# Performance work log

Measured on AMD Instinct MI355X. Metric: run time of the kernel, lower is better.

## Reference

```python
import jax, jax.numpy as jnp
import numpy as np
from math import ceil

N, C_IN, HV, WV = 4, 3, 256, 256
C, K, NUM_LAYERS = 16, 3, 10
HK, WK = 45, 45
PROX_SCALE, KSCALE, KBSCALE, EPS = 10.0, 100.0, 0.01, 1e-8


def conv2_same(x, w):
    # torch F.conv2d (cross-correlation) with 'same' padding
    return jax.lax.conv_general_dilated(x, w, (1, 1), 'SAME',
                                        dimension_numbers=('NCHW', 'OIHW', 'NCHW'))


def pad_to(x, size):
    h, w = x.shape[-2], x.shape[-1]
    pads = [(0, 0)] * (x.ndim - 2) + [(0, size[0] - h), (0, size[1] - w)]
    return jnp.pad(x, pads)


def soft_threshold(x, b):
    return jnp.sign(x) * jax.nn.relu(jnp.abs(x) - b)


def circ_shift(x, s):
    return jnp.roll(x, (-s[0], -s[1]), axis=(-2, -1))


def csq(c):
    return (c * jnp.conj(c)).real


def forward(blurred_image, w0, ws, biases, kernel_biases, kernel_proxes, zetas, eta):
    Nb, C_in, Hv, Wv = blurred_image.shape
    Hs, Ws = Hv + HK - 1, Wv + WK - 1
    Hb, Wb = Hs + HK - 1, Ws + WK - 1
    fft_size = (int(ceil(Hb / 64.0) * 64), int(ceil(Wb / 64.0) * 64))
    rfft = lambda x: jnp.fft.rfft2(x, s=fft_size, axes=(-2, -1))
    irfft = lambda X: jnp.fft.irfft2(X, s=fft_size, axes=(-2, -1))

    # first-layer filter: zero-mean per (out,in) filter, then spatial reflect
    w_mean = w0.reshape(C, C_in, -1).mean(axis=-1)
    w0c = w0 - w_mean[:, :, None, None]
    w0_unreflected = jnp.transpose(w0c, (1, 0, 2, 3))   # (C_in, C, K, K)
    w0r = w0c[:, :, ::-1, ::-1]

    # analysis: cascade of convs, each feature stack padded to fft_size
    wy_list = []
    fy = blurred_image
    for layer in range(NUM_LAYERS):
        w = w0r if layer == 0 else ws[layer - 1]
        fy = conv2_same(fy, w)
        fy_p = pad_to(jnp.pad(fy, ((0, 0), (0, 0), (HK - 1, HK - 1), (WK - 1, WK - 1))), fft_size)
        wy_list.append(fy_p)

    delta = jnp.zeros((Nb, HK, WK), dtype=blurred_image.dtype).at[:, HK // 2, WK // 2].set(1.0)
    b0 = biases[0][None, :, None, None]
    z = soft_threshold(circ_shift(wy_list[-1], (HK // 2, WK // 2)), b0)
    Fz = rfft(z)
    k = delta
    Fg = None
    for layer in range(NUM_LAYERS):
        fy_p = wy_list.pop()
        Ffy = rfft(fy_p)                       # (N, C, H, Wf) complex
        Fk = rfft(k)[:, None]                  # (N, 1, H, Wf)
        zeta = PROX_SCALE * zetas[layer][None, :, None, None]
        num = zeta * (jnp.conj(Fk) * Ffy) + Fz
        den = zeta * csq(Fk) + 1.0
        Fg = num / (den + EPS)
        b = biases[layer + 1][None, :, None, None]
        z = soft_threshold(irfft(Fg), b)
        Fz = rfft(z)
        zk = kernel_proxes[layer]
        num_k = zk * jnp.sum(jnp.conj(Fz) * Ffy, axis=1) + Fk[:, 0]
        den_k = zk * jnp.sum(csq(Fz), axis=1) + 1.0
        k = irfft(num_k / (den_k + EPS))
        k_flat = k.reshape(Nb, -1)
        k_max = jax.scipy.special.logsumexp(k_flat * KSCALE, axis=-1) / KSCALE
        bk = KBSCALE * kernel_biases[layer]
        k = jax.nn.relu(k[:, :HK, :WK] - bk * k_max[:, None, None])
        k_sum = jnp.sum(k, axis=(1, 2), keepdims=True)
        k = (k + EPS * delta) / (k_sum + EPS)

    # final closed-form image solve in frequency domain (3-channel Cramer's rule)
    Fy = rfft(jnp.pad(blurred_image, ((0, 0), (0, 0), (HK - 1, HK - 1), (WK - 1, WK - 1))))
    Fk = rfft(k)                                # (N, H, Wf)
    Fw0 = rfft(circ_shift(pad_to(w0_unreflected, fft_size), (K // 2, K // 2)))  # (C_in, C, H, Wf)
    b_final = biases[NUM_LAYERS + 1][None, :, None, None]
    Fg = rfft(soft_threshold(irfft(Fg), b_final))

    eta_s = PROX_SCALE * eta[None, :, None, None]      # (1, C, 1, 1)
    Fwr, Fwg, Fwb = Fw0[0:1], Fw0[1:2], Fw0[2:3]       # (1, C, H, Wf)
    Fyr, Fyg, Fyb = Fy[:, 0], Fy[:, 1], Fy[:, 2]
    Fk_sq = csq(Fk)
    Crr = Fk_sq + jnp.sum(eta_s * csq(Fwr), axis=1)
    Cgg = Fk_sq + jnp.sum(eta_s * csq(Fwg), axis=1)
    Cbb = Fk_sq + jnp.sum(eta_s * csq(Fwb), axis=1)
    Crg = jnp.sum(eta_s * jnp.conj(Fwr) * Fwg, axis=1)
    Crb = jnp.sum(eta_s * jnp.conj(Fwr) * Fwb, axis=1)
    Cgb = jnp.sum(eta_s * jnp.conj(Fwg) * Fwb, axis=1)
    Fk_conj = jnp.conj(Fk)
    Br = Fk_conj * Fyr + jnp.sum(eta_s * jnp.conj(Fwr) * Fg, axis=1)
    Bg = Fk_conj * Fyg + jnp.sum(eta_s * jnp.conj(Fwg) * Fg, axis=1)
    Bb = Fk_conj * Fyb + jnp.sum(eta_s * jnp.conj(Fwb) * Fg, axis=1)
    Crg_sq, Crb_sq, Cgb_sq = csq(Crg), csq(Crb), csq(Cgb)
    Irr = Cgg * Cbb - Cgb_sq
    Igg = Crr * Cbb - Crb_sq
    Ibb = Crr * Cgg - Crg_sq
    Irg = jnp.conj(Cgb) * Crb - Cbb * Crg
    Irb = Crg * Cgb - Cgg * Crb
    Igb = jnp.conj(Crg) * Crb - Crr * Cgb
    den = (Crr * (Cgg * Cbb - Cgb_sq) - Cgg * Crb_sq - Cbb * Crg_sq
           + 2 * (Crg * Cgb * jnp.conj(Crb)).real) + EPS
    Fxr = Irr * Br + Irg * Bg + Irb * Bb
    Fxg = jnp.conj(Irg) * Br + Igg * Bg + Igb * Bb
    Fxb = jnp.conj(Irb) * Br + jnp.conj(Igb) * Bg + Ibb * Bb
    Fx = jnp.stack([Fxr, Fxg, Fxb], axis=1) / den[:, None]

    image = irfft(Fx)[:, :, HK // 2:HK // 2 + Hv, WK // 2:WK // 2 + Wv]
    return image, k


def setup_inputs() -> dict:
    key = jax.random.key(0)
    ks = jax.random.split(key, 4)

    def xavier(k, shape, fan_in, fan_out):
        std = (2.0 / (fan_in + fan_out)) ** 0.5
        return std * jax.random.normal(k, shape, dtype=jnp.float32)

    return {
        'blurred_image': jax.random.normal(ks[0], (N, C_IN, HV, WV), dtype=jnp.float32),
        'w0': xavier(ks[1], (C, C_IN, K, K), C_IN * K * K, C * K * K),
        'ws': xavier(ks[2], (NUM_LAYERS - 1, C, C, 3, 3), C * 9, C * 9),
        'biases': jnp.full((NUM_LAYERS + 2, C), 0.02, dtype=jnp.float32),
        'kernel_biases': jnp.zeros((NUM_LAYERS,), dtype=jnp.float32),
        'kernel_proxes': jnp.ones((NUM_LAYERS,), dtype=jnp.float32),
        'zetas': jnp.ones((NUM_LAYERS, C), dtype=jnp.float32),
        'eta': jnp.ones((C,), dtype=jnp.float32),
    }


def reference(blurred_image, w0, ws, biases, kernel_biases, kernel_proxes, zetas, eta):
    return forward(blurred_image, w0, ws, biases, kernel_biases, kernel_proxes, zetas, eta)
```

## Files before the change

kernel.cpp:

```cpp
#include <hip/hip_runtime.h>
#include <math.h>

#define FH 384
#define KF 193
#define SPW 147456

typedef __attribute__((ext_vector_type(8))) short short8;
typedef __attribute__((ext_vector_type(4))) float f32x4;
typedef unsigned int u32;
typedef unsigned short u16;

static __device__ __forceinline__ float softt(float v, float b) {
    return copysignf(fmaxf(fabsf(v) - b, 0.f), v);
}
static __device__ __forceinline__ u16 bf16_rn(float v) {
    u32 u = __float_as_uint(v);
    u32 r = (u + 0x7FFFu + ((u >> 16) & 1u)) >> 16;
    return (u16)r;
}
static __device__ __forceinline__ float bf16_to_f(u16 h) {
    return __uint_as_float(((u32)h) << 16);
}
static __device__ __forceinline__ float2 ldc(const uint2* __restrict__ S, size_t i) {
    uint2 u = S[i];
// ... 141 lines not shown
                v = inF ? inF[ii] : (bf16_to_f(iH[ii]) + bf16_to_f(iL[ii]));
            }
            tile[yy][xx] = v;
        }
        __syncthreads();
        float v[9];
#pragma unroll
        for (int dy = 0; dy < 3; dy++)
#pragma unroll
            for (int dx = 0; dx < 3; dx++) v[dy*3+dx] = tile[ty+dy][tx+dx];
#pragma unroll
        for (int co = 0; co < 16; co++) {
            const float* wp = &wl[(co*Cin+ci)*9];
            acc[co] += v[0]*wp[0]+v[1]*wp[1]+v[2]*wp[2]
                     + v[3]*wp[3]+v[4]*wp[4]+v[5]*wp[5]
                     + v[6]*wp[6]+v[7]*wp[7]+v[8]*wp[8];
        }
    }
    int xo = x0 + tx;
    int xd = (xo >> 1) + (xo & 1)*128;
#pragma unroll
    for (int co = 0; co < 16; co++) {
        size_t o = ((size_t)co*256 + (y0+ty))*256 + xd;
        u16 h = bf16_rn(acc[co]);
        oH[o] = h;
        oL[o] = bf16_rn(acc[co] - bf16_to_f(h));
    }
}

__global__ void zinit_kernel(const u16* __restrict__ fy9H, const u16* __restrict__ fy9L,
                             const float* __restrict__ b0,
                             u16* __restrict__ oH, u16* __restrict__ oL, int total)
{
    int idx = blockIdx.x*256 + threadIdx.x;
    if (idx >= total) return;
    int x = idx % FH; int r = idx / FH; int y = r % FH; int plane = r / FH;
    int c = plane & 15;
    int Y = y + 22; if (Y >= FH) Y -= FH;
    int X = x + 22; if (X >= FH) X -= FH;
    int yy = Y - 44, xx = X - 44;
    float v = 0.f;
    if (yy >= 0 && yy < 256 && xx >= 0 && xx < 256) {
        size_t ii = ((size_t)plane*256 + yy)*256 + ((xx>>1) + (xx&1)*128);
        v = bf16_to_f(fy9H[ii]) + bf16_to_f(fy9L[ii]);
    }
    float s = softt(v, b0[c]);
    u16 h = bf16_rn(s);
    size_t d = (size_t)plane*SPW + (size_t)y*FH + ((x>>1) + (x&1)*192);
    oH[d] = h;
    oL[d] = bf16_rn(s - bf16_to_f(h));
}

static __device__ __forceinline__ void r2c192_epilogue(
    f32x4 accA[2][4], f32x4 accB[2][4],
    int col0, int njN, int y0, int wave, int lm, int lq,
    const float2* __restrict__ twT,
    uint2* __restrict__ outp, int B, int plane)
{
#pragma unroll
    for (int mi = 0; mi < 2; ++mi) {
#pragma unroll
        for (int nj = 0; nj < 4; ++nj) {
            if (nj >= njN) continue;
            int n = col0 + nj*16 + lm;
            int j = n >> 1;
            float pA[4], pB[4];
#pragma unroll
            for (int rr = 0; rr < 4; ++rr) {
                pA[rr] = __shfl_xor(accA[mi][nj][rr], 1);
                pB[rr] = __shfl_xor(accB[mi][nj][rr], 1);
            }
            if (((lm & 1) == 0) && j <= 96) {
                float2 tw = twT[j];
                float wr = tw.x, wi = -tw.y;
                int ybase = y0 + wave*32 + mi*16 + lq*4;
#pragma unroll
                for (int rr = 0; rr < 4; ++rr) {
                    float ar = accA[mi][nj][rr], ai = pA[rr];
                    float br = accB[mi][nj][rr], bi = pB[rr];
                    float tr = wr*br - wi*bi;
                    float ti = wr*bi + wi*br;
                    size_t rowb = ((size_t)(ybase+rr)*B + plane)*KF;
                    outp[rowb + j] = packc(ar + tr, ai + ti);
                    if (j < 96) outp[rowb + 192 - j] = packc(ar - tr, -(ai - ti));
                }
            }
        }
    }
}

__global__ __launch_bounds__(256) void r2c192_f(
    const float* __restrict__ inp, int inH, int inW, int inStride, size_t planeStride,
    int offY, int offX,
    const float* __restrict__ thr,
    const u16* __restrict__ TH, const u16* __restrict__ TL,
    const float2* __restrict__ twT,
    uint2* __restrict__ outp, int B)
{
    __shared__ u16 AhS[2][8*64*8];
    __shared__ u16 AlS[2][8*64*8];
    int col0 = blockIdx.x * 64;
    int y0   = blockIdx.y * 128;
    int plane = blockIdx.z;
    int njN = (col0 >= 192) ? 1 : 4;
    int tid = threadIdx.x;
    int wave = tid >> 6, lane = tid & 63;
    int lm = lane & 15, lq = lane >> 4;
    f32x4 accA[2][4], accB[2][4];
#pragma unroll
    for (int mi = 0; mi < 2; ++mi)
#pragma unroll
        for (int nj = 0; nj < 4; ++nj) {
            accA[mi][nj] = (f32x4){0.f,0.f,0.f,0.f};
            accB[mi][nj] = (f32x4){0.f,0.f,0.f,0.f};
        }
    float bthr = thr ? thr[plane & 15] : 0.f;
    const float* inpP = inp + (size_t)plane*planeStride;
    int mhi = (offX + inW) >> 1;
    for (int kt = 0; kt < mhi; kt += 32) {
#pragma unroll
        for (int s = 0; s < 4; ++s) {
            int slot = tid + s*256;
            int r = slot >> 3, kq = slot & 7;
            int yy = y0 + r - offY;
            int xx0 = 2*(kt + kq*4) - offX;
            float v[8];
#pragma unroll
            for (int d = 0; d < 8; ++d) {
                int xx = xx0 + d;
                float t = 0.f;
                if (yy >= 0 && yy < inH && xx >= 0 && xx < inW)
                    t = inpP[(size_t)yy*inStride + xx];
                if (thr) t = softt(t, bthr);
                v[d] = t;
            }
            u16 h[8], l[8];
#pragma unroll
            for (int d = 0; d < 8; ++d) {
                h[d] = bf16_rn(v[d]);
                l[d] = bf16_rn(v[d] - bf16_to_f(h[d]));
            }
            int base = ((r >> 4)*64 + (r & 15) + 16*(kq >> 1))*8 + (kq & 1)*4;
            uint2 w;
            w.x = (u32)h[0] | ((u32)h[2] << 16); w.y = (u32)h[4] | ((u32)h[6] << 16);
            *(uint2*)&AhS[0][base] = w;
            w.x = (u32)h[1] | ((u32)h[3] << 16); w.y = (u32)h[5] | ((u32)h[7] << 16);
            *(uint2*)&AhS[1][base] = w;
            w.x = (u32)l[0] | ((u32)l[2] << 16); w.y = (u32)l[4] | ((u32)l[6] << 16);
            *(uint2*)&AlS[0][base] = w;
            w.x = (u32)l[1] | ((u32)l[3] << 16); w.y = (u32)l[5] | ((u32)l[7] << 16);
            *(uint2*)&AlS[1][base] = w;
        }
        __syncthreads();
        short8 A0h[2], A0l[2], A1h[2], A1l[2];
#pragma unroll
        for (int mi = 0; mi < 2; ++mi) {
            int fo = ((wave*2 + mi)*64 + lane)*8;
            A0h[mi] = *(const short8*)&AhS[0][fo];
            A0l[mi] = *(const short8*)&AlS[0][fo];
            A1h[mi] = *(const short8*)&AhS[1][fo];
            A1l[mi] = *(const short8*)&AlS[1][fo];
        }
#pragma unroll
        for (int nj = 0; nj < 4; ++nj) {
            if (nj >= njN) continue;
            size_t toff = (size_t)(col0 + nj*16 + lm)*192 + kt + lq*8;
            short8 Bh = *(const short8*)(TH + toff);
            short8 Bl = *(const short8*)(TL + toff);
#pragma unroll
            for (int mi = 0; mi < 2; ++mi) {
                accA[mi][nj] = __builtin_amdgcn_mfma_f32_16x16x32_bf16(A0h[mi], Bh, accA[mi][nj], 0, 0, 0);
                accA[mi][nj] = __builtin_amdgcn_mfma_f32_16x16x32_bf16(A0h[mi], Bl, accA[mi][nj], 0, 0, 0);
                accA[mi][nj] = __builtin_amdgcn_mfma_f32_16x16x32_bf16(A0l[mi], Bh, accA[mi][nj], 0, 0, 0);
                accB[mi][nj] = __builtin_amdgcn_mfma_f32_16x16x32_bf16(A1h[mi], Bh, accB[mi][nj], 0, 0, 0);
                accB[mi][nj] = __builtin_amdgcn_mfma_f32_16x16x32_bf16(A1h[mi], Bl, accB[mi][nj], 0, 0, 0);
                accB[mi][nj] = __builtin_amdgcn_mfma_f32_16x16x32_bf16(A1l[mi], Bh, accB[mi][nj], 0, 0, 0);
            }
        }
        __syncthreads();
    }
    r2c192_epilogue(accA, accB, col0, njN, y0, wave, lm, lq, twT, outp, B, plane);
}

__global__ __launch_bounds__(256) void r2c192_s(
    const u16* __restrict__ Hs, const u16* __restrict__ Ls,
    int inH, int inW, int offY, int offX,
    const u16* __restrict__ TH, const u16* __restrict__ TL,
    const float2* __restrict__ twT,
    uint2* __restrict__ outp, int B)
{
    __shared__ u16 AhS[2][8*64*8];
    __shared__ u16 AlS[2][8*64*8];
    int col0 = blockIdx.x * 64;
    int y0   = blockIdx.y * 128;
    int plane = blockIdx.z;
    int njN = (col0 >= 192) ? 1 : 4;
    int tid = threadIdx.x;
    int wave = tid >> 6, lane = tid & 63;
    int lm = lane & 15, lq = lane >> 4;
    f32x4 accA[2][4], accB[2][4];
#pragma unroll
    for (int mi = 0; mi < 2; ++mi)
#pragma unroll
        for (int nj = 0; nj < 4; ++nj) {
            accA[mi][nj] = (f32x4){0.f,0.f,0.f,0.f};
            accB[mi][nj] = (f32x4){0.f,0.f,0.f,0.f};
        }
    const u16* hP = Hs + (size_t)plane*inH*inW;
    const u16* lP = Ls + (size_t)plane*inH*inW;
    int W2  = inW >> 1;
    int ox2 = offX >> 1;
    bool al16 = ((ox2 & 7) == 0);
    int mhi = (offX + inW) >> 1;
    for (int kt = 0; kt < mhi; kt += 32) {
#pragma unroll
        for (int s = 0; s < 4; ++s) {
            int slot = tid + s*256;
            int p    = slot >> 9;
            int inr  = slot & 511;
            int r = inr >> 2, kq2 = inr & 3;
            int yy = y0 + r - offY;
            int m0 = kt + kq2*8;
            int pos = m0 - ox2;
            uint4 hq = {0u,0u,0u,0u}, lq4 = {0u,0u,0u,0u};
            if (yy >= 0 && yy < inH) {
                const u16* hr = hP + (size_t)yy*inW + (size_t)p*W2;
                const u16* lr = lP + (size_t)yy*inW + (size_t)p*W2;
                if (pos >= 0 && pos + 8 <= W2) {
                    if (al16) {
                        hq  = *(const uint4*)(hr + pos);
                        lq4 = *(const uint4*)(lr + pos);
                    } else {
                        hq.x = *(const u32*)(hr+pos);   hq.y = *(const u32*)(hr+pos+2);
                        hq.z = *(const u32*)(hr+pos+4); hq.w = *(const u32*)(hr+pos+6);
                        lq4.x = *(const u32*)(lr+pos);   lq4.y = *(const u32*)(lr+pos+2);
                        lq4.z = *(const u32*)(lr+pos+4); lq4.w = *(const u32*)(lr+pos+6);
                    }
                } else if (pos + 8 > 0 && pos < W2) {
#pragma unroll
                    for (int q = 0; q < 4; ++q) {
                        int pp = pos + 2*q;
                        if (pp >= 0 && pp + 2 <= W2) {
                            ((u32*)&hq)[q]  = *(const u32*)(hr+pp);
                            ((u32*)&lq4)[q] = *(const u32*)(lr+pp);
                        }
                    }
                }
            }
            int base = ((r >> 4)*64 + (r & 15) + 16*kq2)*8;
            *(uint4*)&AhS[p][base] = hq;
            *(uint4*)&AlS[p][base] = lq4;
        }
        __syncthreads();
        short8 A0h[2], A0l[2], A1h[2], A1l[2];
#pragma unroll
        for (int mi = 0; mi < 2; ++mi) {
            int fo = ((wave*2 + mi)*64 + lane)*8;
            A0h[mi] = *(const short8*)&AhS[0][fo];
            A0l[mi] = *(const short8*)&AlS[0][fo];
            A1h[mi] = *(const short8*)&AhS[1][fo];
            A1l[mi] = *(const short8*)&AlS[1][fo];
        }
#pragma unroll
        for (int nj = 0; nj < 4; ++nj) {
            if (nj >= njN) continue;
            size_t toff = (size_t)(col0 + nj*16 + lm)*192 + kt + lq*8;
            short8 Bh = *(const short8*)(TH + toff);
            short8 Bl = *(const short8*)(TL + toff);
#pragma unroll
            for (int mi = 0; mi < 2; ++mi) {
                accA[mi][nj] = __builtin_amdgcn_mfma_f32_16x16x32_bf16(A0h[mi], Bh, accA[mi][nj], 0, 0, 0);
                accA[mi][nj] = __builtin_amdgcn_mfma_f32_16x16x32_bf16(A0h[mi], Bl, accA[mi][nj], 0, 0, 0);
                accA[mi][nj] = __builtin_amdgcn_mfma_f32_16x16x32_bf16(A0l[mi], Bh, accA[mi][nj], 0, 0, 0);
                accB[mi][nj] = __builtin_amdgcn_mfma_f32_16x16x32_bf16(A1h[mi], Bh, accB[mi][nj], 0, 0, 0);
                accB[mi][nj] = __builtin_amdgcn_mfma_f32_16x16x32_bf16(A1h[mi], Bl, accB[mi][nj], 0, 0, 0);
                accB[mi][nj] = __builtin_amdgcn_mfma_f32_16x16x32_bf16(A1l[mi], Bh, accB[mi][nj], 0, 0, 0);
            }
        }
        __syncthreads();
    }
    r2c192_epilogue(accA, accB, col0, njN, y0, wave, lm, lq, twT, outp, B, plane);
}

__device__ __forceinline__ void lse_comb(float& m, float& s, float m2, float s2)
{
    if (m2 > m) { s = s * expf(m - m2) + s2; m = m2; }
    else        { s = s + s2 * expf(m2 - m); }
}

__global__ void gpm_kernel(uint2* __restrict__ S, const float2* __restrict__ twT, int rows)
{
    int idx = blockIdx.x*256 + threadIdx.x;
    if (idx >= rows * 97) return;
    int j = idx % 97;
    size_t b = (size_t)(idx / 97) * KF;
    if (j == 96) {
        float2 f = ldc(S, b + 96);
        S[b + 96] = packc(2.f*f.x, -2.f*f.y);
    } else {
        float2 f1 = ldc(S, b + j);
        float2 f2 = ldc(S, b + 192 - j);
        float gpx = f1.x + f2.x, gpy = f1.y - f2.y;
        float hx  = f1.x - f2.x, hy  = f1.y + f2.y;
        float2 tw = twT[j];
        float gmx = tw.x*hx - tw.y*hy;
        float gmy = tw.x*hy + tw.y*hx;
        S[b + j]       = packc(gpx, gpy);
        S[b + 192 - j] = packc(gmx, gmy);
    }
}

template<bool FUSE_LSE>
__global__ __launch_bounds__(256) void c2r192(
    const uint2* __restrict__ Ain,
    const u16* __restrict__ UH, const u16* __restrict__ UL,
    float* __restrict__ outp, const float* __restrict__ thr,
    u16* __restrict__ spH, u16* __restrict__ spL, int B,
    float2* __restrict__ parts)
{
    __shared__ u16 AhS[2][8*64*8];
    __shared__ u16 AlS[2][8*64*8];
    int col0 = blockIdx.x * 64;
    int y0   = blockIdx.y * 128;
    int plane = blockIdx.z;
    int tid = threadIdx.x;
    int wave = tid >> 6, lane = tid & 63;
    int lm = lane & 15, lq = lane >> 4;
    f32x4 accP[2][4], accQ[2][4];
#pragma unroll
    for (int mi = 0; mi < 2; ++mi)
#pragma unroll
        for (int nj = 0; nj < 4; ++nj) {
            accP[mi][nj] = (f32x4){0.f,0.f,0.f,0.f};
            accQ[mi][nj] = (f32x4){0.f,0.f,0.f,0.f};
        }
    for (int kt = 0; kt < 194; kt += 32) {
#pragma unroll
        for (int s = 0; s < 8; ++s) {
            int slot = tid + s*256;
            int p   = slot >> 10;
            int inr = slot & 1023;
            int r = inr >> 3, kq = inr & 7;
            size_t rowb = ((size_t)(y0 + r)*B + plane)*KF;
            int j0 = (kt + kq*4) >> 1;
            uint2 u0, u1;
            u0.x = u0.y = u1.x = u1.y = 0u;
            if (p == 0) {
                if (j0 < 96) u0 = Ain[rowb + j0];
                else if (j0 == 96) {
                    uint2 t = Ain[rowb + 96];
                    u0.x = t.x & 0xffffu; u0.y = t.y & 0xffffu;
                }
                if (j0 + 1 < 96) u1 = Ain[rowb + j0 + 1];
            } else {
                if (j0 < 96) u0 = Ain[rowb + 192 - j0];
                else if (j0 == 96) {
                    uint2 t = Ain[rowb + 96];
                    u0.x = t.x >> 16; u0.y = t.y >> 16;
                }
                if (j0 + 1 < 96) u1 = Ain[rowb + 191 - j0];
            }
            int base = ((r >> 4)*64 + (r & 15) + 16*(kq >> 1))*8 + (kq & 1)*4;
            uint2 hp, lp;
            hp.x = u0.x; hp.y = u1.x;
            lp.x = u0.y; lp.y = u1.y;
            *(uint2*)&AhS[p][base] = hp;
            *(uint2*)&AlS[p][base] = lp;
        }
        __syncthreads();
        short8 A0h[2], A0l[2], A1h[2], A1l[2];
#pragma unroll
        for (int mi = 0; mi < 2; ++mi) {
            int fo = ((wave*2 + mi)*64 + lane)*8;
            A0h[mi] = *(const short8*)&AhS[0][fo];
            A0l[mi] = *(const short8*)&AlS[0][fo];
            A1h[mi] = *(const short8*)&AhS[1][fo];
            A1l[mi] = *(const short8*)&AlS[1][fo];
        }
#pragma unroll
        for (int nj = 0; nj < 4; ++nj) {
            size_t toff = (size_t)(col0 + nj*16 + lm)*224 + kt + lq*8;
            short8 Bh = *(const short8*)(UH + toff);
            short8 Bl = *(const short8*)(UL + toff);
#pragma unroll
            for (int mi = 0; mi < 2; ++mi) {
                accP[mi][nj] = __builtin_amdgcn_mfma_f32_16x16x32_bf16(A0h[mi], Bh, accP[mi][nj], 0, 0, 0);
                accP[mi][nj] = __builtin_amdgcn_mfma_f32_16x16x32_bf16(A0h[mi], Bl, accP[mi][nj], 0, 0, 0);
                accP[mi][nj] = __builtin_amdgcn_mfma_f32_16x16x32_bf16(A0l[mi], Bh, accP[mi][nj], 0, 0, 0);
                accQ[mi][nj] = __builtin_amdgcn_mfma_f32_16x16x32_bf16(A1h[mi], Bh, accQ[mi][nj], 0, 0, 0);
                accQ[mi][nj] = __builtin_amdgcn_mfma_f32_16x16x32_bf16(A1h[mi], Bl, accQ[mi][nj], 0, 0, 0);
                accQ[mi][nj] = __builtin_amdgcn_mfma_f32_16x16x32_bf16(A1l[mi], Bh, accQ[mi][nj], 0, 0, 0);
            }
        }
        __syncthreads();
    }
    float bthr = thr ? thr[plane & 15] : 0.f;
    float lm_ = -1e30f, ls_ = 0.f;
#pragma unroll
    for (int mi = 0; mi < 2; ++mi) {
#pragma unroll
        for (int nj = 0; nj < 4; ++nj) {
            int m = col0 + nj*16 + lm;
#pragma unroll
            for (int rr = 0; rr < 4; ++rr) {
                int y = y0 + wave*32 + mi*16 + lq*4 + rr;
                float xe = accP[mi][nj][rr];
                float xo = accQ[mi][nj][rr];
                float2 o2; o2.x = xe; o2.y = xo;
                *(float2*)&outp[((size_t)plane*FH + y)*FH + 2*m] = o2;
                if (spH) {
                    float s0 = softt(xe, bthr), s1 = softt(xo, bthr);
                    u16 h0 = bf16_rn(s0), h1 = bf16_rn(s1);
                    u16 l0 = bf16_rn(s0 - bf16_to_f(h0)), l1 = bf16_rn(s1 - bf16_to_f(h1));
                    size_t d = (size_t)plane*SPW + (size_t)y*FH + m;
                    spH[d]       = h0; spL[d]       = l0;
                    spH[d + 192] = h1; spL[d + 192] = l1;
                }
                if (FUSE_LSE) {
                    lse_comb(lm_, ls_, 100.f*xe, 1.f);
                    lse_comb(lm_, ls_, 100.f*xo, 1.f);
                }
            }
        }
    }
    if (FUSE_LSE) {
        __shared__ float sm[256], ss[256];
        sm[tid] = lm_; ss[tid] = ls_;
        __syncthreads();
        for (int st = 128; st > 0; st >>= 1) {
            if (tid < st) {
                float mm = sm[tid], sc = ss[tid];
                lse_comb(mm, sc, sm[tid+st], ss[tid+st]);
                sm[tid] = mm; ss[tid] = sc;
            }
            __syncthreads();
        }
        if (tid == 0) {
            float2 o; o.x = sm[0]; o.y = ss[0];
            parts[plane*9 + blockIdx.y*3 + blockIdx.x] = o;
        }
    }
}

template<bool FUSE_FG>
__global__ __launch_bounds__(384) void zgemm_col_mfma8(
    const u16* __restrict__ EH, const u16* __restrict__ EL,
    const uint2* __restrict__ Bm, uint2* __restrict__ Cm, int N, float sgn,
    int ktHi, const float2* __restrict__ twT,
    uint2* __restrict__ FzFg, const uint2* __restrict__ FkB,
    const float* __restrict__ zet16, int GKF)
{
    __shared__ u16 BhS[8][2*64*8];
    __shared__ u16 BlS[8][2*64*8];
    int col0 = blockIdx.x * 32;
    int tid = threadIdx.x;
    int wave = tid >> 6, lane = tid & 63;
    int lm = lane & 15, lq = lane >> 4;
    f32x4 acc[8][2];
#pragma unroll
    for (int p = 0; p < 8; ++p)
#pragma unroll
        for (int nj = 0; nj < 2; ++nj)
            acc[p][nj] = (f32x4){0.f,0.f,0.f,0.f};
    int arow = wave*16 + lm;
    for (int kt = 0; kt < ktHi; kt += 32) {
        int tbase = kt >> 1;
#pragma unroll
        for (int s = 0; s < 6; ++s) {
            int slot = tid + s*384;
            if (slot < 2048) {
                int p    = slot >> 8;
                int inr  = slot & 255;
                int pair = inr >> 5;
                int n    = inr & 31;
                int gn   = col0 + n;
                int t0   = tbase + pair*2;
                uint2 u0, u1;
                u0.x = u0.y = u1.x = u1.y = 0u;
                if (gn < N) {
                    u0 = Bm[(size_t)(8*t0 + p)*N + gn];
                    u1 = Bm[(size_t)(8*t0 + 8 + p)*N + gn];
                }
                int ntile = n >> 4, n0 = n & 15;
                int lrow  = (pair >> 1)*16 + n0;
                int base  = (ntile*64 + lrow)*8 + (pair & 1)*4;
                uint2 hp, lp;
                hp.x = u0.x; hp.y = u1.x;
                lp.x = u0.y; lp.y = u1.y;
                *(uint2*)&BhS[p][base] = hp;
                *(uint2*)&BlS[p][base] = lp;
            }
        }
// ... 92 lines not shown
                        float den = zeta*(fk.x*fk.x + fk.y*fk.y) + 1.f + 1e-8f;
                        float inv = 1.f/den;
                        FzFg[(size_t)row*N + coln] = packc(nx*inv, ny*inv);
                    }
                }
            }
        }
    }
}

__global__ void knum_kernel(const uint2* __restrict__ Fz, const uint2* __restrict__ Ffy,
                            const uint2* __restrict__ Fk, const float* __restrict__ kprox,
                            int L, int total, uint2* __restrict__ outk)
{
    int idx = blockIdx.x*256 + threadIdx.x;
    if (idx >= total) return;
    int k = idx % KF; int r = idx / KF;
    float zk = kprox[L];
    float s1x = 0.f, s1y = 0.f, s2 = 0.f;
    for (int c = 0; c < 16; ++c) {
        size_t bi = ((size_t)r*16 + c)*KF + k;
        float2 fz = ldc(Fz, bi), fy = ldc(Ffy, bi);
        s1x += fz.x*fy.x + fz.y*fy.y;
        s1y += fz.x*fy.y - fz.y*fy.x;
        s2  += fz.x*fz.x + fz.y*fz.y;
    }
    float2 fk = ldc(Fk, idx);
    float nx = zk*s1x + fk.x, ny = zk*s1y + fk.y;
    float den = zk*s2 + 1.f + 1e-8f;
    float inv = 1.f/den;
    outk[idx] = packc(nx*inv, ny*inv);
}

__global__ void zero_kernel(float* __restrict__ p, int n)
{
    int i = blockIdx.x*256 + threadIdx.x;
    if (i < n) p[i] = 0.f;
}

__global__ void kdelta_kernel(float* __restrict__ kful, int G)
{
    int t = threadIdx.x;
    if (t < G) kful[(size_t)t*FH*FH + 22*FH + 22] = 1.f;
}

__global__ __launch_bounds__(256) void knew_kernel(const float2* __restrict__ parts,
    const float* __restrict__ kraw0, const float* __restrict__ kb, int L,
    float* __restrict__ kful0)
{
    int img = blockIdx.x;
    const float* kraw = kraw0 + (size_t)img*FH*FH;
    float*       kful = kful0 + (size_t)img*FH*FH;
    int t = threadIdx.x;
    __shared__ float sm[16], ss[16];
    if (t < 16) {
        if (t < 9) { float2 p = parts[img*9 + t]; sm[t] = p.x; ss[t] = p.y; }
        else       { sm[t] = -1e30f; ss[t] = 0.f; }
    }
    __syncthreads();
    for (int st = 8; st > 0; st >>= 1) {
        if (t < st) {
            float mm = sm[t], sc = ss[t];
            lse_comb(mm, sc, sm[t+st], ss[t+st]);
            sm[t] = mm; ss[t] = sc;
        }
        __syncthreads();
    }
    float kmax = (sm[0] + logf(ss[0])) * 0.01f;
    float thr = 0.01f * kb[L] * kmax;
    float vs[8]; float loc = 0.f;
#pragma unroll
    for (int ii = 0; ii < 8; ++ii) {
        int i = t + ii*256;
        float v = 0.f;
        if (i < 45*45) {
            int y = i/45, x = i - y*45;
            v = fmaxf(kraw[y*FH + x] - thr, 0.f);
        }
        vs[ii] = v; loc += v;
    }
    __shared__ float sr[256];
    sr[t] = loc; __syncthreads();
    for (int st = 128; st > 0; st >>= 1) { if (t < st) sr[t] += sr[t+st]; __syncthreads(); }
    float den = sr[0] + 1e-8f;
#pragma unroll
    for (int ii = 0; ii < 8; ++ii) {
        int i = t + ii*256;
        if (i < 45*45) {
            int y = i/45, x = i - y*45;
            float v = vs[ii] + ((y == 22 && x == 22) ? 1e-8f : 0.f);
            kful[y*FH + x] = v / den;
        }
    }
}

__global__ void fw0_kernel(const float* __restrict__ w0c, const float2* __restrict__ Ef,
                           float2* __restrict__ Fw0)
{
    int idx = blockIdx.x*256 + threadIdx.x;
    if (idx >= 48*FH*KF) return;
    int k = idx % KF; int r = idx / KF;
    int c = r & 15; int r2 = r >> 4;
    int ci = r2 % 3; int h = r2 / 3;
    float accx = 0.f, accy = 0.f;
#pragma unroll
    for (int ky = 0; ky < 3; ++ky) {
        int a1 = ky - 1; if (a1 < 0) a1 += FH;
        float2 e1 = Ef[h*FH + a1];
#pragma unroll
        for (int kx = 0; kx < 3; ++kx) {
            int a2 = kx - 1; if (a2 < 0) a2 += FH;
            float2 e2 = Ef[k*FH + a2];
            float wv = w0c[((c*3 + ci)*3 + ky)*3 + kx];
// ... 130 lines not shown
    auto alloc = [&](size_t bytes) -> void* {
        void* p = (void*)(base + off);
        off += (bytes + 255) & ~(size_t)255;
        return p;
    };
    float2* Ef   = (float2*)alloc((size_t)FH*FH*8);
    float2* twT  = (float2*)alloc(384*8);
    u16* EfH = (u16*)alloc((size_t)96*96*2);
    u16* EfL = (u16*)alloc((size_t)96*96*2);
    u16* EiH = (u16*)alloc((size_t)96*96*2);
    u16* EiL = (u16*)alloc((size_t)96*96*2);
    u16* T1H = (u16*)alloc((size_t)208*192*2);
    u16* T1L = (u16*)alloc((size_t)208*192*2);
    u16* U1H = (u16*)alloc((size_t)192*224*2);
    u16* U1L = (u16*)alloc((size_t)192*224*2);
    float*  w0cB = (float*)alloc(432*4);
    u16*    fyH  = (u16*)alloc((size_t)10*G*16*65536*2);
    u16*    fyL  = (u16*)alloc((size_t)10*G*16*65536*2);
    float*  zsp  = (float*)alloc((size_t)G*16*FH*FH*4);
    u16*    zspSH= (u16*)alloc((size_t)G*16*SPW*2);
    u16*    zspSL= (u16*)alloc((size_t)G*16*SPW*2);
    uint2*  mid  = (uint2*)alloc((size_t)G*16*FH*KF*8);
    uint2*  FzFg = (uint2*)alloc((size_t)G*16*FH*KF*8);
    uint2*  Ffy  = (uint2*)alloc((size_t)G*16*FH*KF*8);
    uint2*  Fk   = (uint2*)alloc((size_t)G*FH*KF*8);
    uint2*  kfA  = (uint2*)alloc((size_t)G*FH*KF*8);
    uint2*  kfB  = (uint2*)alloc((size_t)G*FH*KF*8);
    uint2*  kmid = (uint2*)alloc((size_t)G*FH*KF*8);
    float*  kraw = (float*)alloc((size_t)G*FH*FH*4);
    float*  kful = (float*)alloc((size_t)G*FH*FH*4);
    uint2*  FyB  = (uint2*)alloc((size_t)G*3*FH*KF*8);
    uint2*  FxB  = (uint2*)alloc((size_t)G*3*FH*KF*8);
    float2* lseP = (float2*)alloc((size_t)G*64*8);
    float2* Fw0B = (float2*)fyH;

    init_ef_k<<<(FH*FH+255)/256, 256, 0, stream>>>(Ef);
    init_tw<<<2, 256, 0, stream>>>(twT);
    init_e48<<<(96*96+255)/256, 256, 0, stream>>>(EfH, EfL, 0);
    init_e48<<<(96*96+255)/256, 256, 0, stream>>>(EiH, EiL, 1);
    init_t192<<<(208*192+255)/256, 256, 0, stream>>>(T1H, T1L);
    init_u192<<<(192*224+255)/256, 256, 0, stream>>>(U1H, U1L);
    w0c_kernel<<<1, 64, 0, stream>>>(w0, w0cB);

    auto zgf = [&](const uint2* Bm, uint2* Cm, int Ncols) {
        zgemm_col_mfma8<false><<<dim3((Ncols+31)/32), 384, 0, stream>>>(
            EfH, EfL, Bm, Cm, Ncols, -1.f, 96, twT, nullptr, nullptr, nullptr, 0);
    };
    auto zgi = [&](const uint2* Bm, uint2* Cm, int Ncols) {
        zgemm_col_mfma8<false><<<dim3((Ncols+31)/32), 384, 0, stream>>>(
            EiH, EiL, Bm, Cm, Ncols, 1.f, 96, twT, nullptr, nullptr, nullptr, 0);
    };
    auto r2c = [&](const float* inp, int inH, int inW, int oY, int oX,
                   const float* thr, uint2* o, int B) {
        r2c192_f<<<dim3(4, 3, B), 256, 0, stream>>>(
            inp, inH, inW, inW, (size_t)inH*inW, oY, oX, thr, T1H, T1L, twT, o, B);
    };
    auto r2cs = [&](const u16* Hs, const u16* Ls, int inH, int inW, int oY, int oX,
                    uint2* o, int B) {
        r2c192_s<<<dim3(4, 3, B), 256, 0, stream>>>(
            Hs, Ls, inH, inW, oY, oX, T1H, T1L, twT, o, B);
    };
    auto c2r = [&](uint2* Ain, float* o, int B,
                   const float* thr, u16* sH, u16* sL) {
        int rows = FH * B;
        gpm_kernel<<<(rows*97 + 255)/256, 256, 0, stream>>>(Ain, twT, rows);
        c2r192<false><<<dim3(3, 3, B), 256, 0, stream>>>(
            Ain, U1H, U1L, o, thr, sH, sL, B, nullptr);
    };
    auto c2rk = [&](uint2* Ain, float* o, int B, float2* parts) {
        int rows = FH * B;
        gpm_kernel<<<(rows*97 + 255)/256, 256, 0, stream>>>(Ain, twT, rows);
        c2r192<true><<<dim3(3, 3, B), 256, 0, stream>>>(
            Ain, U1H, U1L, o, nullptr, nullptr, nullptr, B, parts);
    };
    auto r2ck = [&]() {
        r2c192_f<<<dim3(4, 1, G), 256, 0, stream>>>(
            kful, 45, 45, FH, (size_t)FH*FH, 0, 0, nullptr, T1H, T1L, twT, kmid, G);
        zgemm_col_mfma8<false><<<dim3((G*KF+31)/32), 384, 0, stream>>>(
            EfH, EfL, kmid, Fk, G*KF, -1.f, 32, twT, nullptr, nullptr, nullptr, 0);
    };

    const size_t CKL = (size_t)G*16*65536;

    for (int g0 = 0; g0 < 4; g0 += G) {
        const float* img = blurred + (size_t)g0*3*65536;

        conv3x3_kernel<<<dim3(16,16,G), 256, 0, stream>>>(
            img, nullptr, nullptr, w0cB, fyH, fyL, 3, 1, (size_t)3*65536);
        for (int l = 1; l < 10; ++l)
            conv3x3_kernel<<<dim3(16,16,G), 256, 0, stream>>>(
                nullptr, fyH + (size_t)(l-1)*CKL, fyL + (size_t)(l-1)*CKL,
                wsw + (size_t)(l-1)*2304,
                fyH + (size_t)l*CKL, fyL + (size_t)l*CKL, 16, 0, (size_t)16*65536);

        int totZ = G*16*FH*FH;
        zinit_kernel<<<(totZ+255)/256, 256, 0, stream>>>(
            fyH + 9*CKL, fyL + 9*CKL, biases, zspSH, zspSL, totZ);
        r2cs(zspSH, zspSL, FH, FH, 0, 0, mid, G*16);
        zgf(mid, FzFg, G*16*KF);

        zero_kernel<<<(G*FH*FH+255)/256, 256, 0, stream>>>(kful, G*FH*FH);
        kdelta_kernel<<<1, 64, 0, stream>>>(kful, G);

        int totK = G*FH*KF;
        int NS = G*16*KF;
        for (int it = 0; it < 10; ++it) {
            int Lfy = 9 - it;
            r2ck();
            r2cs(fyH + (size_t)Lfy*CKL, fyL + (size_t)Lfy*CKL, 256, 256, 44, 44, mid, G*16);
            zgemm_col_mfma8<true><<<dim3((NS+31)/32), 384, 0, stream>>>(
                EfH, EfL, mid, Ffy, NS, -1.f, 96, twT,
                FzFg, Fk, zetas + it*16, G*KF);
            zgi(FzFg, mid, NS);
            c2r(mid, zsp, G*16, biases + (it+1)*16, zspSH, zspSL);
            r2cs(zspSH, zspSL, FH, FH, 0, 0, mid, G*16);
            zgf(mid, FzFg, NS);
            knum_kernel<<<(totK+255)/256, 256, 0, stream>>>(FzFg, Ffy, Fk, kprox, it, totK, kfA);
            zgi(kfA, kfB, G*KF);
            c2rk(kfB, kraw, G, lseP);
            knew_kernel<<<G, 256, 0, stream>>>(lseP, kraw, kbias, it, kful);
        }

        r2c(img, 256, 256, 44, 44, nullptr, mid, 3*G);
        zgf(mid, FyB, 3*G*KF);
        r2ck();
        r2c(zsp, FH, FH, 0, 0, biases + 11*16, mid, G*16);
        zgf(mid, FzFg, G*16*KF);
        fw0_kernel<<<(48*FH*KF+255)/256, 256, 0, stream>>>(w0cB, Ef, Fw0B);
        wiener_kernel<<<(totK+255)/256, 256, 0, stream>>>(Fk, FyB, Fw0B, FzFg, eta, G, totK, FxB);
// ... 9 lines not shown
```

Baseline: 7.612 ms.

## Retile row DFT GEMM kernels so each block covers all output columns

The r2c192 and c2r192 MFMA kernels now give each 512-thread block a full 128-row stripe with every output column (13 or 12 column tiles per wave). Each wave owns 16 rows and reuses its A fragments across all column tiles. This removes the column dimension of the grid, so the A tile is staged and bf16-split once per row stripe rather than once per column block, and the padded fourth column block goes away. In exchange the grid is several times smaller, which may leave many CUs idle. Register pressure also rises from 26 accumulators per thread, and the LSE partial-reduction indexing is changed to three parts per plane.

```diff
diff --git a/kernel.cpp b/kernel.cpp
--- a/kernel.cpp
+++ b/kernel.cpp
@@ -217,44 +217,40 @@
 }
 
 static __device__ __forceinline__ void r2c192_epilogue(
-    f32x4 accA[2][4], f32x4 accB[2][4],
-    int col0, int njN, int y0, int wave, int lm, int lq,
+    f32x4 accA[13], f32x4 accB[13],
+    int y0, int wave, int lm, int lq,
     const float2* __restrict__ twT,
     uint2* __restrict__ outp, int B, int plane)
 {
 #pragma unroll
-    for (int mi = 0; mi < 2; ++mi) {
-#pragma unroll
-        for (int nj = 0; nj < 4; ++nj) {
-            if (nj >= njN) continue;
-            int n = col0 + nj*16 + lm;
-            int j = n >> 1;
-            float pA[4], pB[4];
+    for (int nj = 0; nj < 13; ++nj) {
+        int n = nj*16 + lm;
+        int j = n >> 1;
+        float pA[4], pB[4];
+#pragma unroll
+        for (int rr = 0; rr < 4; ++rr) {
+            pA[rr] = __shfl_xor(accA[nj][rr], 1);
+            pB[rr] = __shfl_xor(accB[nj][rr], 1);
+        }
+        if (((lm & 1) == 0) && j <= 96) {
+            float2 tw = twT[j];
+            float wr = tw.x, wi = -tw.y;
+            int ybase = y0 + wave*16 + lq*4;
 #pragma unroll
             for (int rr = 0; rr < 4; ++rr) {
-                pA[rr] = __shfl_xor(accA[mi][nj][rr], 1);
-                pB[rr] = __shfl_xor(accB[mi][nj][rr], 1);
-            }
-            if (((lm & 1) == 0) && j <= 96) {
-                float2 tw = twT[j];
-                float wr = tw.x, wi = -tw.y;
-                int ybase = y0 + wave*32 + mi*16 + lq*4;
-#pragma unroll
-                for (int rr = 0; rr < 4; ++rr) {
-                    float ar = accA[mi][nj][rr], ai = pA[rr];
-                    float br = accB[mi][nj][rr], bi = pB[rr];
-                    float tr = wr*br - wi*bi;
-                    float ti = wr*bi + wi*br;
-                    size_t rowb = ((size_t)(ybase+rr)*B + plane)*KF;
-                    outp[rowb + j] = packc(ar + tr, ai + ti);
-                    if (j < 96) outp[rowb + 192 - j] = packc(ar - tr, -(ai - ti));
-                }
-            }
-        }
-    }
-}
-
-__global__ __launch_bounds__(256) void r2c192_f(
+                float ar = accA[nj][rr], ai = pA[rr];
+                float br = accB[nj][rr], bi = pB[rr];
+                float tr = wr*br - wi*bi;
+                float ti = wr*bi + wi*br;
+                size_t rowb = ((size_t)(ybase+rr)*B + plane)*KF;
+                outp[rowb + j] = packc(ar + tr, ai + ti);
+                if (j < 96) outp[rowb + 192 - j] = packc(ar - tr, -(ai - ti));
+            }
+        }
+    }
+}
+
+__global__ __launch_bounds__(512) void r2c192_f(
     const float* __restrict__ inp, int inH, int inW, int inStride, size_t planeStride,
     int offY, int offX,
     const float* __restrict__ thr,
@@ -264,28 +260,24 @@
 {
     __shared__ u16 AhS[2][8*64*8];
     __shared__ u16 AlS[2][8*64*8];
-    int col0 = blockIdx.x * 64;
-    int y0   = blockIdx.y * 128;
-    int plane = blockIdx.z;
-    int njN = (col0 >= 192) ? 1 : 4;
+    int y0   = blockIdx.x * 128;
+    int plane = blockIdx.y;
     int tid = threadIdx.x;
     int wave = tid >> 6, lane = tid & 63;
     int lm = lane & 15, lq = lane >> 4;
-    f32x4 accA[2][4], accB[2][4];
-#pragma unroll
-    for (int mi = 0; mi < 2; ++mi)
-#pragma unroll
-        for (int nj = 0; nj < 4; ++nj) {
-            accA[mi][nj] = (f32x4){0.f,0.f,0.f,0.f};
-            accB[mi][nj] = (f32x4){0.f,0.f,0.f,0.f};
-        }
+    f32x4 accA[13], accB[13];
+#pragma unroll
+    for (int nj = 0; nj < 13; ++nj) {
+        accA[nj] = (f32x4){0.f,0.f,0.f,0.f};
+        accB[nj] = (f32x4){0.f,0.f,0.f,0.f};
+    }
     float bthr = thr ? thr[plane & 15] : 0.f;
     const float* inpP = inp + (size_t)plane*planeStride;
     int mhi = (offX + inW) >> 1;
     for (int kt = 0; kt < mhi; kt += 32) {
 #pragma unroll
-        for (int s = 0; s < 4; ++s) {
-            int slot = tid + s*256;
+        for (int s = 0; s < 2; ++s) {
+            int slot = tid + s*512;
             int r = slot >> 3, kq = slot & 7;
             int yy = y0 + r - offY;
             int xx0 = 2*(kt + kq*4) - offX;
@@ -317,37 +309,32 @@
             *(uint2*)&AlS[1][base] = w;
         }
         __syncthreads();
-        short8 A0h[2], A0l[2], A1h[2], A1l[2];
-#pragma unroll
-        for (int mi = 0; mi < 2; ++mi) {
-            int fo = ((wave*2 + mi)*64 + lane)*8;
-            A0h[mi] = *(const short8*)&AhS[0][fo];
-            A0l[mi] = *(const short8*)&AlS[0][fo];
-            A1h[mi] = *(const short8*)&AhS[1][fo];
-            A1l[mi] = *(const short8*)&AlS[1][fo];
-        }
-#pragma unroll
-        for (int nj = 0; nj < 4; ++nj) {
-            if (nj >= njN) continue;
-            size_t toff = (size_t)(col0 + nj*16 + lm)*192 + kt + lq*8;
+        short8 A0h, A0l, A1h, A1l;
+        {
+            int fo = (wave*64 + lane)*8;
+            A0h = *(const short8*)&AhS[0][fo];
+            A0l = *(const short8*)&AlS[0][fo];
+            A1h = *(const short8*)&AhS[1][fo];
+            A1l = *(const short8*)&AlS[1][fo];
+        }
+#pragma unroll
+        for (int nj = 0; nj < 13; ++nj) {
+            size_t toff = (size_t)(nj*16 + lm)*192 + kt + lq*8;
             short8 Bh = *(const short8*)(TH + toff);
             short8 Bl = *(const short8*)(TL + toff);
-#pragma unroll
-            for (int mi = 0; mi < 2; ++mi) {
-                accA[mi][nj] = __builtin_amdgcn_mfma_f32_16x16x32_bf16(A0h[mi], Bh, accA[mi][nj], 0, 0, 0);
-                accA[mi][nj] = __builtin_amdgcn_mfma_f32_16x16x32_bf16(A0h[mi], Bl, accA[mi][nj], 0, 0, 0);
-                accA[mi][nj] = __builtin_amdgcn_mfma_f32_16x16x32_bf16(A0l[mi], Bh, accA[mi][nj], 0, 0, 0);
-                accB[mi][nj] = __builtin_amdgcn_mfma_f32_16x16x32_bf16(A1h[mi], Bh, accB[mi][nj], 0, 0, 0);
-                accB[mi][nj] = __builtin_amdgcn_mfma_f32_16x16x32_bf16(A1h[mi], Bl, accB[mi][nj], 0, 0, 0);
-                accB[mi][nj] = __builtin_amdgcn_mfma_f32_16x16x32_bf16(A1l[mi], Bh, accB[mi][nj], 0, 0, 0);
-            }
-        }
-        __syncthreads();
-    }
-    r2c192_epilogue(accA, accB, col0, njN, y0, wave, lm, lq, twT, outp, B, plane);
-}
-
-__global__ __launch_bounds__(256) void r2c192_s(
+            accA[nj] = __builtin_amdgcn_mfma_f32_16x16x32_bf16(A0h, Bh, accA[nj], 0, 0, 0);
+            accA[nj] = __builtin_amdgcn_mfma_f32_16x16x32_bf16(A0h, Bl, accA[nj], 0, 0, 0);
+            accA[nj] = __builtin_amdgcn_mfma_f32_16x16x32_bf16(A0l, Bh, accA[nj], 0, 0, 0);
+            accB[nj] = __builtin_amdgcn_mfma_f32_16x16x32_bf16(A1h, Bh, accB[nj], 0, 0, 0);
+            accB[nj] = __builtin_amdgcn_mfma_f32_16x16x32_bf16(A1h, Bl, accB[nj], 0, 0, 0);
+            accB[nj] = __builtin_amdgcn_mfma_f32_16x16x32_bf16(A1l, Bh, accB[nj], 0, 0, 0);
+        }
+        __syncthreads();
+    }
+    r2c192_epilogue(accA, accB, y0, wave, lm, lq, twT, outp, B, plane);
+}
+
+__global__ __launch_bounds__(512) void r2c192_s(
     const u16* __restrict__ Hs, const u16* __restrict__ Ls,
     int inH, int inW, int offY, int offX,
     const u16* __restrict__ TH, const u16* __restrict__ TL,
@@ -356,21 +343,17 @@
 {
     __shared__ u16 AhS[2][8*64*8];
     __shared__ u16 AlS[2][8*64*8];
-    int col0 = blockIdx.x * 64;
-    int y0   = blockIdx.y * 128;
-    int plane = blockIdx.z;
-    int njN = (col0 >= 192) ? 1 : 4;
+    int y0   = blockIdx.x * 128;
+    int plane = blockIdx.y;
     int tid = threadIdx.x;
     int wave = tid >> 6, lane = tid & 63;
     int lm = lane & 15, lq = lane >> 4;
-    f32x4 accA[2][4], accB[2][4];
-#pragma unroll
-    for (int mi = 0; mi < 2; ++mi)
-#pragma unroll
-        for (int nj = 0; nj < 4; ++nj) {
-            accA[mi][nj] = (f32x4){0.f,0.f,0.f,0.f};
-            accB[mi][nj] = (f32x4){0.f,0.f,0.f,0.f};
-        }
+    f32x4 accA[13], accB[13];
+#pragma unroll
+    for (int nj = 0; nj < 13; ++nj) {
+        accA[nj] = (f32x4){0.f,0.f,0.f,0.f};
+        accB[nj] = (f32x4){0.f,0.f,0.f,0.f};
+    }
     const u16* hP = Hs + (size_t)plane*inH*inW;
     const u16* lP = Ls + (size_t)plane*inH*inW;
     int W2  = inW >> 1;
@@ -379,8 +362,8 @@
     int mhi = (offX + inW) >> 1;
     for (int kt = 0; kt < mhi; kt += 32) {
 #pragma unroll
-        for (int s = 0; s < 4; ++s) {
-            int slot = tid + s*256;
+        for (int s = 0; s < 2; ++s) {
+            int slot = tid + s*512;
             int p    = slot >> 9;
             int inr  = slot & 511;
             int r = inr >> 2, kq2 = inr & 3;
@@ -417,34 +400,29 @@
             *(uint4*)&AlS[p][base] = lq4;
         }
         __syncthreads();
-        short8 A0h[2], A0l[2], A1h[2], A1l[2];
-#pragma unroll
-        for (int mi = 0; mi < 2; ++mi) {
-            int fo = ((wave*2 + mi)*64 + lane)*8;
-            A0h[mi] = *(const short8*)&AhS[0][fo];
-            A0l[mi] = *(const short8*)&AlS[0][fo];
-            A1h[mi] = *(const short8*)&AhS[1][fo];
-            A1l[mi] = *(const short8*)&AlS[1][fo];
-        }
-#pragma unroll
-        for (int nj = 0; nj < 4; ++nj) {
-            if (nj >= njN) continue;
-            size_t toff = (size_t)(col0 + nj*16 + lm)*192 + kt + lq*8;
+        short8 A0h, A0l, A1h, A1l;
+        {
+            int fo = (wave*64 + lane)*8;
+            A0h = *(const short8*)&AhS[0][fo];
+            A0l = *(const short8*)&AlS[0][fo];
+            A1h = *(const short8*)&AhS[1][fo];
+            A1l = *(const short8*)&AlS[1][fo];
+        }
+#pragma unroll
+        for (int nj = 0; nj < 13; ++nj) {
+            size_t toff = (size_t)(nj*16 + lm)*192 + kt + lq*8;
             short8 Bh = *(const short8*)(TH + toff);
             short8 Bl = *(const short8*)(TL + toff);
-#pragma unroll
-            for (int mi = 0; mi < 2; ++mi) {
-                accA[mi][nj] = __builtin_amdgcn_mfma_f32_16x16x32_bf16(A0h[mi], Bh, accA[mi][nj], 0, 0, 0);
-                accA[mi][nj] = __builtin_amdgcn_mfma_f32_16x16x32_bf16(A0h[mi], Bl, accA[mi][nj], 0, 0, 0);
-                accA[mi][nj] = __builtin_amdgcn_mfma_f32_16x16x32_bf16(A0l[mi], Bh, accA[mi][nj], 0, 0, 0);
-                accB[mi][nj] = __builtin_amdgcn_mfma_f32_16x16x32_bf16(A1h[mi], Bh, accB[mi][nj], 0, 0, 0);
-                accB[mi][nj] = __builtin_amdgcn_mfma_f32_16x16x32_bf16(A1h[mi], Bl, accB[mi][nj], 0, 0, 0);
-                accB[mi][nj] = __builtin_amdgcn_mfma_f32_16x16x32_bf16(A1l[mi], Bh, accB[mi][nj], 0, 0, 0);
-            }
-        }
-        __syncthreads();
-    }
-    r2c192_epilogue(accA, accB, col0, njN, y0, wave, lm, lq, twT, outp, B, plane);
+            accA[nj] = __builtin_amdgcn_mfma_f32_16x16x32_bf16(A0h, Bh, accA[nj], 0, 0, 0);
+            accA[nj] = __builtin_amdgcn_mfma_f32_16x16x32_bf16(A0h, Bl, accA[nj], 0, 0, 0);
+            accA[nj] = __builtin_amdgcn_mfma_f32_16x16x32_bf16(A0l, Bh, accA[nj], 0, 0, 0);
+            accB[nj] = __builtin_amdgcn_mfma_f32_16x16x32_bf16(A1h, Bh, accB[nj], 0, 0, 0);
+            accB[nj] = __builtin_amdgcn_mfma_f32_16x16x32_bf16(A1h, Bl, accB[nj], 0, 0, 0);
+            accB[nj] = __builtin_amdgcn_mfma_f32_16x16x32_bf16(A1l, Bh, accB[nj], 0, 0, 0);
+        }
+        __syncthreads();
+    }
+    r2c192_epilogue(accA, accB, y0, wave, lm, lq, twT, outp, B, plane);
 }
 
 __device__ __forceinline__ void lse_comb(float& m, float& s, float m2, float s2)
@@ -476,7 +454,7 @@
 }
 
 template<bool FUSE_LSE>
-__global__ __launch_bounds__(256) void c2r192(
+__global__ __launch_bounds__(512) void c2r192(
     const uint2* __restrict__ Ain,
     const u16* __restrict__ UH, const u16* __restrict__ UL,
     float* __restrict__ outp, const float* __restrict__ thr,
@@ -485,24 +463,21 @@
 {
     __shared__ u16 AhS[2][8*64*8];
     __shared__ u16 AlS[2][8*64*8];
-    int col0 = blockIdx.x * 64;
-    int y0   = blockIdx.y * 128;
-    int plane = blockIdx.z;
+    int y0   = blockIdx.x * 128;
+    int plane = blockIdx.y;
     int tid = threadIdx.x;
     int wave = tid >> 6, lane = tid & 63;
     int lm = lane & 15, lq = lane >> 4;
-    f32x4 accP[2][4], accQ[2][4];
-#pragma unroll
-    for (int mi = 0; mi < 2; ++mi)
-#pragma unroll
-        for (int nj = 0; nj < 4; ++nj) {
-            accP[mi][nj] = (f32x4){0.f,0.f,0.f,0.f};
-            accQ[mi][nj] = (f32x4){0.f,0.f,0.f,0.f};
-        }
+    f32x4 accP[12], accQ[12];
+#pragma unroll
+    for (int nj = 0; nj < 12; ++nj) {
+        accP[nj] = (f32x4){0.f,0.f,0.f,0.f};
+        accQ[nj] = (f32x4){0.f,0.f,0.f,0.f};
+    }
     for (int kt = 0; kt < 194; kt += 32) {
 #pragma unroll
-        for (int s = 0; s < 8; ++s) {
-            int slot = tid + s*256;
+        for (int s = 0; s < 4; ++s) {
+            int slot = tid + s*512;
             int p   = slot >> 10;
             int inr = slot & 1023;
             int r = inr >> 3, kq = inr & 7;
@@ -533,66 +508,59 @@
             *(uint2*)&AlS[p][base] = lp;
         }
         __syncthreads();
-        short8 A0h[2], A0l[2], A1h[2], A1l[2];
-#pragma unroll
-        for (int mi = 0; mi < 2; ++mi) {
-            int fo = ((wave*2 + mi)*64 + lane)*8;
-            A0h[mi] = *(const short8*)&AhS[0][fo];
-            A0l[mi] = *(const short8*)&AlS[0][fo];
-            A1h[mi] = *(const short8*)&AhS[1][fo];
-            A1l[mi] = *(const short8*)&AlS[1][fo];
-        }
-#pragma unroll
-        for (int nj = 0; nj < 4; ++nj) {
-            size_t toff = (size_t)(col0 + nj*16 + lm)*224 + kt + lq*8;
+        short8 A0h, A0l, A1h, A1l;
+        {
+            int fo = (wave*64 + lane)*8;
+            A0h = *(const short8*)&AhS[0][fo];
+            A0l = *(const short8*)&AlS[0][fo];
+            A1h = *(const short8*)&AhS[1][fo];
+            A1l = *(const short8*)&AlS[1][fo];
+        }
+#pragma unroll
+        for (int nj = 0; nj < 12; ++nj) {
+            size_t toff = (size_t)(nj*16 + lm)*224 + kt + lq*8;
             short8 Bh = *(const short8*)(UH + toff);
             short8 Bl = *(const short8*)(UL + toff);
-#pragma unroll
-            for (int mi = 0; mi < 2; ++mi) {
-                accP[mi][nj] = __builtin_amdgcn_mfma_f32_16x16x32_bf16(A0h[mi], Bh, accP[mi][nj], 0, 0, 0);
-                accP[mi][nj] = __builtin_amdgcn_mfma_f32_16x16x32_bf16(A0h[mi], Bl, accP[mi][nj], 0, 0, 0);
-                accP[mi][nj] = __builtin_amdgcn_mfma_f32_16x16x32_bf16(A0l[mi], Bh, accP[mi][nj], 0, 0, 0);
-                accQ[mi][nj] = __builtin_amdgcn_mfma_f32_16x16x32_bf16(A1h[mi], Bh, accQ[mi][nj], 0, 0, 0);
-                accQ[mi][nj] = __builtin_amdgcn_mfma_f32_16x16x32_bf16(A1h[mi], Bl, accQ[mi][nj], 0, 0, 0);
-                accQ[mi][nj] = __builtin_amdgcn_mfma_f32_16x16x32_bf16(A1l[mi], Bh, accQ[mi][nj], 0, 0, 0);
-            }
+            accP[nj] = __builtin_amdgcn_mfma_f32_16x16x32_bf16(A0h, Bh, accP[nj], 0, 0, 0);
+            accP[nj] = __builtin_amdgcn_mfma_f32_16x16x32_bf16(A0h, Bl, accP[nj], 0, 0, 0);
+            accP[nj] = __builtin_amdgcn_mfma_f32_16x16x32_bf16(A0l, Bh, accP[nj], 0, 0, 0);
+            accQ[nj] = __builtin_amdgcn_mfma_f32_16x16x32_bf16(A1h, Bh, accQ[nj], 0, 0, 0);
+            accQ[nj] = __builtin_amdgcn_mfma_f32_16x16x32_bf16(A1h, Bl, accQ[nj], 0, 0, 0);
+            accQ[nj] = __builtin_amdgcn_mfma_f32_16x16x32_bf16(A1l, Bh, accQ[nj], 0, 0, 0);
         }
         __syncthreads();
     }
     float bthr = thr ? thr[plane & 15] : 0.f;
     float lm_ = -1e30f, ls_ = 0.f;
 #pragma unroll
-    for (int mi = 0; mi < 2; ++mi) {
-#pragma unroll
-        for (int nj = 0; nj < 4; ++nj) {
-            int m = col0 + nj*16 + lm;
-#pragma unroll
-            for (int rr = 0; rr < 4; ++rr) {
-                int y = y0 + wave*32 + mi*16 + lq*4 + rr;
-                float xe = accP[mi][nj][rr];
-                float xo = accQ[mi][nj][rr];
-                float2 o2; o2.x = xe; o2.y = xo;
-                *(float2*)&outp[((size_t)plane*FH + y)*FH + 2*m] = o2;
-                if (spH) {
-                    float s0 = softt(xe, bthr), s1 = softt(xo, bthr);
-                    u16 h0 = bf16_rn(s0), h1 = bf16_rn(s1);
-                    u16 l0 = bf16_rn(s0 - bf16_to_f(h0)), l1 = bf16_rn(s1 - bf16_to_f(h1));
-                    size_t d = (size_t)plane*SPW + (size_t)y*FH + m;
-                    spH[d]       = h0; spL[d]       = l0;
-                    spH[d + 192] = h1; spL[d + 192] = l1;
-                }
-                if (FUSE_LSE) {
-                    lse_comb(lm_, ls_, 100.f*xe, 1.f);
-                    lse_comb(lm_, ls_, 100.f*xo, 1.f);
-                }
+    for (int nj = 0; nj < 12; ++nj) {
+        int m = nj*16 + lm;
+#pragma unroll
+        for (int rr = 0; rr < 4; ++rr) {
+            int y = y0 + wave*16 + lq*4 + rr;
+            float xe = accP[nj][rr];
+            float xo = accQ[nj][rr];
+            float2 o2; o2.x = xe; o2.y = xo;
+            *(float2*)&outp[((size_t)plane*FH + y)*FH + 2*m] = o2;
+            if (spH) {
+                float s0 = softt(xe, bthr), s1 = softt(xo, bthr);
+                u16 h0 = bf16_rn(s0), h1 = bf16_rn(s1);
+                u16 l0 = bf16_rn(s0 - bf16_to_f(h0)), l1 = bf16_rn(s1 - bf16_to_f(h1));
+                size_t d = (size_t)plane*SPW + (size_t)y*FH + m;
+                spH[d]       = h0; spL[d]       = l0;
+                spH[d + 192] = h1; spL[d + 192] = l1;
+            }
+            if (FUSE_LSE) {
+                lse_comb(lm_, ls_, 100.f*xe, 1.f);
+                lse_comb(lm_, ls_, 100.f*xo, 1.f);
             }
         }
     }
     if (FUSE_LSE) {
-        __shared__ float sm[256], ss[256];
+        __shared__ float sm[512], ss[512];
         sm[tid] = lm_; ss[tid] = ls_;
         __syncthreads();
-        for (int st = 128; st > 0; st >>= 1) {
+        for (int st = 256; st > 0; st >>= 1) {
             if (tid < st) {
                 float mm = sm[tid], sc = ss[tid];
                 lse_comb(mm, sc, sm[tid+st], ss[tid+st]);
@@ -602,7 +570,7 @@
         }
         if (tid == 0) {
             float2 o; o.x = sm[0]; o.y = ss[0];
-            parts[plane*9 + blockIdx.y*3 + blockIdx.x] = o;
+            parts[plane*3 + blockIdx.x] = o;
         }
     }
 }
@@ -801,13 +769,13 @@
     const float* kraw = kraw0 + (size_t)img*FH*FH;
     float*       kful = kful0 + (size_t)img*FH*FH;
     int t = threadIdx.x;
-    __shared__ float sm[16], ss[16];
-    if (t < 16) {
-        if (t < 9) { float2 p = parts[img*9 + t]; sm[t] = p.x; ss[t] = p.y; }
+    __shared__ float sm[4], ss[4];
+    if (t < 4) {
+        if (t < 3) { float2 p = parts[img*3 + t]; sm[t] = p.x; ss[t] = p.y; }
         else       { sm[t] = -1e30f; ss[t] = 0.f; }
     }
     __syncthreads();
-    for (int st = 8; st > 0; st >>= 1) {
+    for (int st = 2; st > 0; st >>= 1) {
         if (t < st) {
             float mm = sm[t], sc = ss[t];
             lse_comb(mm, sc, sm[t+st], ss[t+st]);
@@ -1044,29 +1012,29 @@
     };
     auto r2c = [&](const float* inp, int inH, int inW, int oY, int oX,
                    const float* thr, uint2* o, int B) {
-        r2c192_f<<<dim3(4, 3, B), 256, 0, stream>>>(
+        r2c192_f<<<dim3(3, B), 512, 0, stream>>>(
             inp, inH, inW, inW, (size_t)inH*inW, oY, oX, thr, T1H, T1L, twT, o, B);
     };
     auto r2cs = [&](const u16* Hs, const u16* Ls, int inH, int inW, int oY, int oX,
                     uint2* o, int B) {
-        r2c192_s<<<dim3(4, 3, B), 256, 0, stream>>>(
+        r2c192_s<<<dim3(3, B), 512, 0, stream>>>(
             Hs, Ls, inH, inW, oY, oX, T1H, T1L, twT, o, B);
     };
     auto c2r = [&](uint2* Ain, float* o, int B,
                    const float* thr, u16* sH, u16* sL) {
         int rows = FH * B;
         gpm_kernel<<<(rows*97 + 255)/256, 256, 0, stream>>>(Ain, twT, rows);
-        c2r192<false><<<dim3(3, 3, B), 256, 0, stream>>>(
+        c2r192<false><<<dim3(3, B), 512, 0, stream>>>(
             Ain, U1H, U1L, o, thr, sH, sL, B, nullptr);
     };
     auto c2rk = [&](uint2* Ain, float* o, int B, float2* parts) {
         int rows = FH * B;
         gpm_kernel<<<(rows*97 + 255)/256, 256, 0, stream>>>(Ain, twT, rows);
-        c2r192<true><<<dim3(3, 3, B), 256, 0, stream>>>(
+        c2r192<true><<<dim3(3, B), 512, 0, stream>>>(
             Ain, U1H, U1L, o, nullptr, nullptr, nullptr, B, parts);
     };
     auto r2ck = [&]() {
-        r2c192_f<<<dim3(4, 1, G), 256, 0, stream>>>(
+        r2c192_f<<<dim3(1, G), 512, 0, stream>>>(
             kful, 45, 45, FH, (size_t)FH*FH, 0, 0, nullptr, T1H, T1L, twT, kmid, G);
         zgemm_col_mfma8<false><<<dim3((G*KF+31)/32), 384, 0, stream>>>(
             EfH, EfL, kmid, Fk, G*KF, -1.f, 32, twT, nullptr, nullptr, nullptr, 0);
```

Result: slower. 8.930 ms (+17.3%).
